# Performance work log

Hardware: AMD Instinct MI355X
Metric: run time of the kernel (lower is better)

## Reference

```python
import jax, jax.numpy as jnp
import numpy as np

N_E = 8192
E_DIM = 256
BETA = 0.25
ORTHO_COEF = 1.0


def setup_inputs() -> dict:
    key = jax.random.key(0)
    k1, k2 = jax.random.split(key)
    z = jax.random.normal(k1, (16, E_DIM, 32, 32), dtype=jnp.float32)
    # nn.Embedding init: uniform(-1/n_e, 1/n_e)
    codebook = jax.random.uniform(k2, (N_E, E_DIM), dtype=jnp.float32,
                                  minval=-1.0 / N_E, maxval=1.0 / N_E)
    return {"z": z, "codebook": codebook}


def reference(z, codebook):
    B, C, H, W = z.shape
    n_e = codebook.shape[0]
    zt = jnp.transpose(z, (0, 2, 3, 1))            # (B,H,W,C)
    zf = zt.reshape(-1, C)                          # (N,C)

    # L2 distances: ||z||^2 + ||e||^2 - 2 z.e
    d = (jnp.sum(zf * zf, axis=1, keepdims=True)
         + jnp.sum(codebook * codebook, axis=1)
         - 2.0 * jnp.matmul(zf, codebook.T))        # (N, n_e)
    idx = jnp.argmin(d, axis=1)                     # (N,)

    z_q_flat = codebook[idx]                        # gather == one-hot @ codebook
    z_q = z_q_flat.reshape(zt.shape)                # (B,H,W,C)

    sg = jax.lax.stop_gradient
    loss = (BETA * jnp.mean((sg(z_q) - zt) ** 2)
            + jnp.mean((z_q - sg(zt)) ** 2))

    # ortho regularizer (force_emb_len_1 == False branch)
    wn = codebook / jnp.linalg.norm(codebook, axis=1, keepdims=True)
    diff = jnp.matmul(wn, wn.T) - jnp.eye(n_e, dtype=codebook.dtype)
    ortho_reg_term = ORTHO_COEF * jnp.sum(diff ** 2) / (n_e ** 2)

    # straight-through estimator
    z_q_st = zt + sg(z_q - zt)

    # perplexity from mean one-hot usage
    N = zf.shape[0]
    counts = jnp.zeros((n_e,), dtype=zt.dtype).at[idx].add(1.0)
    e_mean = counts / N
    perplexity = jnp.exp(-jnp.sum(e_mean * jnp.log(e_mean + 1e-10)))

    z_q_out = jnp.transpose(z_q_st, (0, 3, 1, 2))   # (B,C,H,W)
    return z_q_out, loss, ortho_reg_term, perplexity, idx
```

## Files before the change

### kernel.cpp

```cpp
#include <hip/hip_runtime.h>
#include <hip/hip_bf16.h>
#include <math.h>


#define N_E     8192
#define C_DIM   256
#define N_VEC   16384
#define N_ELEM  4194304
#define MARGIN  6.0e-4f

#define WS_COUNTS   0
#define WS_M        32768
#define WS_ACCUM    294912
#define WS_LISTLEN  294944
#define WS_ZERO_BYTES 295200
#define WS_CE       295200
#define WS_RN       327968
#define WS_A        360736
#define WS_KEYS     426272
#define WS_LISTS    557344
#define WS_TILEMIN  4751648
#define WS_ZBF      8945952
#define WS_CBBF     17334560
#define WS_THR      21528864
#define WS_ZT       21594400

typedef short short8v __attribute__((ext_vector_type(8)));
typedef float f32x4  __attribute__((ext_vector_type(4)));

__device__ inline unsigned short f2bf(float f) {
    unsigned int x = __float_as_uint(f);
    return (unsigned short)((x + 0x7fffu + ((x >> 16) & 1u)) >> 16);
}

__device__ inline void gload16(const void* g, void* l) {
    __builtin_amdgcn_global_load_lds(
        (const __attribute__((address_space(1))) unsigned int*)g,
        (__attribute__((address_space(3))) unsigned int*)l, 16, 0, 0);
}

__global__ __launch_bounds__(256) void k_cbprep(const float* __restrict__ cb,
                                                float* __restrict__ ce,
                                                float* __restrict__ rn,
                                                unsigned short* __restrict__ cbbf) {
    int j = blockIdx.x;
    int tid = threadIdx.x;
    float v = cb[(size_t)j * C_DIM + tid];
    cbbf[(size_t)j * C_DIM + tid] = f2bf(v);
    float s = v * v;
    #pragma unroll
    for (int off = 32; off > 0; off >>= 1) s += __shfl_down(s, off, 64);
    __shared__ float sh[4];
    if ((tid & 63) == 0) sh[tid >> 6] = s;
    __syncthreads();
    if (tid == 0) {
        float t = sh[0] + sh[1] + sh[2] + sh[3];
        ce[j] = t;
        rn[j] = 1.0f / sqrtf(t);
    }
}

__global__ __launch_bounds__(256) void k_ztrans(const float* __restrict__ z,
                                                unsigned short* __restrict__ zbf,
                                                float* __restrict__ zT,
                                                float* __restrict__ A) {
    __shared__ float tile[64 * 260];
    const int tid = threadIdx.x;
    const int n0 = blockIdx.x * 64;
    const int b = n0 >> 10, hw0 = n0 & 1023;
    const float* zp = z + (size_t)b * 262144 + hw0;

    const int hw = tid & 63, cg = tid >> 6;
    #pragma unroll 8
    for (int p = 0; p < 64; ++p) {
        int c = p * 4 + cg;
        tile[hw * 260 + c] = zp[(size_t)c * 1024 + hw];
    }
    __syncthreads();

    if (tid < 64) {
        float a = 0.0f;
        #pragma unroll 8
        for (int c = 0; c < C_DIM; ++c) {
            float v = tile[tid * 260 + c];
            a = fmaf(v, v, a);
        }
        A[n0 + tid] = a;
    }

    const int r = tid >> 2, q = tid & 3;
    unsigned short* dst = zbf + (size_t)(n0 + r) * C_DIM + q * 64;
    float* dstT         = zT  + (size_t)(n0 + r) * C_DIM + q * 64;
    const float* src = &tile[r * 260 + q * 64];
    #pragma unroll
    for (int i = 0; i < 8; ++i) {
        f32x4 lo = *(const f32x4*)&src[i * 8];
        f32x4 hi = *(const f32x4*)&src[i * 8 + 4];
        *(f32x4*)&dstT[i * 8]     = lo;
        *(f32x4*)&dstT[i * 8 + 4] = hi;
        short8v u;
        #pragma unroll
        for (int x = 0; x < 4; ++x) { u[x] = (short)f2bf(lo[x]); u[4 + x] = (short)f2bf(hi[x]); }
        *(short8v*)(dst + i * 8) = u;
    }
}

__global__ __launch_bounds__(256) void k_mfma(const unsigned short* __restrict__ zbf,
                                              const unsigned short* __restrict__ cbbf,
                                              const float* __restrict__ cb,
                                              const float* __restrict__ rn,
                                              float* __restrict__ tilemin,
                                              float* __restrict__ M) {
    __shared__ unsigned long long ldsraw[4352];
    const int tid = threadIdx.x;

    if (blockIdx.x < 8192) {
        unsigned short* As = (unsigned short*)ldsraw;
        unsigned short* Bs = As + 128 * 64;
        float (*smin)[2]   = (float(*)[2])(Bs + 128 * 64);

        const int lin = blockIdx.x;
        const int x = lin & 7, r = lin >> 3;
        const int jp = r >> 7, q = r & 127;
        const int by = x * 16 + (q >> 3), bx = jp * 8 + (q & 7);
        const int n0 = by * 128, j0 = bx * 128;
        const int wave = tid >> 6, lane = tid & 63;
        const int wx = wave & 1, wy = wave >> 1;
        const int g = lane >> 4, c = lane & 15;

        const int lrow  = lane >> 3;
        const int lslot = (lane & 7) ^ lrow;
        const int rbase = wave * 32;

        f32x4 acc[4][4];
        #pragma unroll
        for (int i = 0; i < 4; ++i)
            #pragma unroll
            for (int j = 0; j < 4; ++j) acc[i][j] = (f32x4){0.f, 0.f, 0.f, 0.f};

        for (int kc = 0; kc < C_DIM; kc += 64) {
            __syncthreads();
            #pragma unroll
            for (int i = 0; i < 4; ++i) {
                const int row8 = rbase + i * 8;
                const unsigned short* ga =
                    zbf  + (size_t)(n0 + row8 + lrow) * C_DIM + kc + lslot * 8;
                const unsigned short* gb =
                    cbbf + (size_t)(j0 + row8 + lrow) * C_DIM + kc + lslot * 8;
                gload16(ga, &As[row8 * 64]);
                gload16(gb, &Bs[row8 * 64]);
            }
            __syncthreads();

            #pragma unroll
            for (int kk = 0; kk < 2; ++kk) {
                short8v a[4], b[4];
                #pragma unroll
                for (int f = 0; f < 4; ++f) {
                    const int row = wy * 64 + f * 16 + c;
                    a[f] = *(const short8v*)&As[row * 64 + (((kk * 4 + g) ^ (c & 7)) * 8)];
                }
                #pragma unroll
                for (int f = 0; f < 4; ++f) {
                    const int row = wx * 64 + f * 16 + c;
                    b[f] = *(const short8v*)&Bs[row * 64 + (((kk * 4 + g) ^ (c & 7)) * 8)];
                }
                #pragma unroll
                for (int nf = 0; nf < 4; ++nf)
                    #pragma unroll
                    for (int jf = 0; jf < 4; ++jf)
                        acc[nf][jf] = __builtin_amdgcn_mfma_f32_16x16x32_bf16(
                            a[nf], b[jf], acc[nf][jf], 0, 0, 0);
            }
        }

        #pragma unroll
        for (int nf = 0; nf < 4; ++nf) {
            #pragma unroll
            for (int rr = 0; rr < 4; ++rr) {
                float mx = acc[nf][0][rr];
                #pragma unroll
                for (int jf = 1; jf < 4; ++jf) mx = fmaxf(mx, acc[nf][jf][rr]);
                #pragma unroll
                for (int off = 1; off < 16; off <<= 1)
                    mx = fmaxf(mx, __shfl_xor(mx, off, 64));
                if (c == 0) smin[wy * 64 + nf * 16 + g * 4 + rr][wx] = -2.0f * mx;
            }
        }
        __syncthreads();
        if (tid < 128)
            tilemin[(size_t)bx * N_VEC + n0 + tid] = fminf(smin[tid][0], smin[tid][1]);

    } else {
        float* aT = (float*)ldsraw;
        float* bT = aT + 64 * 68;
        const int gidx = blockIdx.x - 8192;
        const int k0 = (gidx & 3) * 64, l0 = ((gidx >> 2) & 3) * 64;
        const int jc0 = (gidx >> 4) * 256;
        const int tk = tid & 15, tl = tid >> 4;
        float acc[4][4];
        #pragma unroll
        for (int i = 0; i < 4; ++i)
            #pragma unroll
            for (int l = 0; l < 4; ++l) acc[i][l] = 0.0f;

        for (int jc = jc0; jc < jc0 + 256; jc += 64) {
            __syncthreads();
            {
                int kk = tid & 63, jj0 = tid >> 6;
                #pragma unroll
                for (int p = 0; p < 16; ++p) {
                    int jj = p * 4 + jj0;
                    float rr = rn[jc + jj];
                    const float* row = cb + (size_t)(jc + jj) * C_DIM;
                    aT[jj * 68 + kk] = row[k0 + kk] * rr;
                    bT[jj * 68 + kk] = row[l0 + kk] * rr;
                }
            }
            __syncthreads();
            #pragma unroll 8
            for (int jj = 0; jj < 64; ++jj) {
                float4 av = *(const float4*)&aT[jj * 68 + tk * 4];
                float4 bv = *(const float4*)&bT[jj * 68 + tl * 4];
                float a4[4] = {av.x, av.y, av.z, av.w};
                float b4[4] = {bv.x, bv.y, bv.z, bv.w};
                #pragma unroll
                for (int i = 0; i < 4; ++i)
                    #pragma unroll
                    for (int l = 0; l < 4; ++l)
                        acc[i][l] = fmaf(a4[i], b4[l], acc[i][l]);
            }
        }
        #pragma unroll
        for (int i = 0; i < 4; ++i)
            #pragma unroll
            for (int l = 0; l < 4; ++l)
                atomicAdd(&M[(size_t)(k0 + tk * 4 + i) * C_DIM + l0 + tl * 4 + l], acc[i][l]);
    }
}

__global__ __launch_bounds__(256) void k_rowmin(const float* __restrict__ tilemin,
                                               float* __restrict__ thr,
                                               unsigned long long* __restrict__ keys) {
    __shared__ float red[4][64];
    const int nl = threadIdx.x & 63, tg = threadIdx.x >> 6;
    const int n = blockIdx.x * 64 + nl;
    float m = 3.4e38f;
    #pragma unroll
    for (int i = 0; i < 16; ++i)
        m = fminf(m, tilemin[(size_t)(tg * 16 + i) * N_VEC + n]);
    red[tg][nl] = m;
    __syncthreads();
    if (tg == 0) {
        thr[n] = fminf(fminf(red[0][nl], red[1][nl]),
                       fminf(red[2][nl], red[3][nl])) + MARGIN;
        keys[n] = ~0ull;
    }
}

__global__ __launch_bounds__(256) void k_build(const float* __restrict__ tilemin,
                                               const float* __restrict__ thr,
                                               int* __restrict__ listlen,
                                               int* __restrict__ lists) {
    const int t = blockIdx.x;
    const int lane = threadIdx.x & 63;
    #pragma unroll
    for (int it = 0; it < 8; ++it) {
        int n = blockIdx.y * 2048 + it * 256 + threadIdx.x;
        bool qq = tilemin[(size_t)t * N_VEC + n] <= thr[n];
        unsigned long long mask = __ballot(qq);
        if (mask) {
            int ldr = __ffsll(mask) - 1;
            int base = 0;
            if (lane == ldr) base = atomicAdd(&listlen[t], __popcll(mask));
            base = __shfl(base, ldr, 64);
            if (qq) {
                int pre = __popcll(mask & ((1ull << lane) - 1ull));
                lists[t * N_VEC + base + pre] = n;
            }
        }
    }
}

__global__ __launch_bounds__(256) void k_refine2(const float* __restrict__ zT,
                                                 const float* __restrict__ cb,
                                                 const float* __restrict__ ce,
                                                 const float* __restrict__ A,
                                                 const int* __restrict__ listlen,
                                                 const int* __restrict__ lists,
                                                 unsigned long long* __restrict__ keys) {
    __shared__ float e_s[128 * 68];
    __shared__ float z_s[32 * 68];
    __shared__ int   rows_s[32];

    const int t = blockIdx.x;
    const int len = listlen[t];
    const int tid = threadIdx.x;
    const int jg = tid & 31, rg = tid >> 5;
    const int j0 = t * 128;

    for (int b0 = blockIdx.y * 32; b0 < len; b0 += 128 * 32) {
        const int nrows = min(32, len - b0);
        __syncthreads();
        if (tid < 32)
            rows_s[tid] = lists[t * N_VEC + b0 + min(tid, nrows - 1)];

        float acc[4][4];
        #pragma unroll
        for (int rr = 0; rr < 4; ++rr)
            #pragma unroll
            for (int jj = 0; jj < 4; ++jj) acc[rr][jj] = 0.0f;

        for (int kc = 0; kc < C_DIM; kc += 64) {
            __syncthreads();
            {
                int jr = tid >> 1, ko = (tid & 1) * 32;
                #pragma unroll
                for (int i = 0; i < 8; ++i)
                    *(float4*)&e_s[jr * 68 + ko + i * 4] =
                        *(const float4*)&cb[(size_t)(j0 + jr) * C_DIM + kc + ko + i * 4];
            }
            {
                int r = tid >> 3, ko = (tid & 7) * 8;
                const float* zp = &zT[(size_t)rows_s[r] * C_DIM + kc + ko];
                *(float4*)&z_s[r * 68 + ko]     = *(const float4*)&zp[0];
                *(float4*)&z_s[r * 68 + ko + 4] = *(const float4*)&zp[4];
            }
            __syncthreads();

            #pragma unroll
            for (int k4 = 0; k4 < 16; ++k4) {
                float4 ef[4], zf[4];
                #pragma unroll
                for (int jj = 0; jj < 4; ++jj)
                    ef[jj] = *(const float4*)&e_s[(jg + 32 * jj) * 68 + k4 * 4];
                #pragma unroll
                for (int rr = 0; rr < 4; ++rr)
                    zf[rr] = *(const float4*)&z_s[(rg * 4 + rr) * 68 + k4 * 4];
                #pragma unroll
                for (int kk = 0; kk < 4; ++kk)
                    #pragma unroll
                    for (int rr = 0; rr < 4; ++rr)
                        #pragma unroll
                        for (int jj = 0; jj < 4; ++jj)
                            acc[rr][jj] = fmaf(((const float*)&zf[rr])[kk],
                                               ((const float*)&ef[jj])[kk], acc[rr][jj]);
            }
        }

        #pragma unroll
        for (int rr = 0; rr < 4; ++rr) {
            const int n = rows_s[rg * 4 + rr];
            const float An = A[n];
            unsigned long long best = ~0ull;
            #pragma unroll
            for (int jj = 0; jj < 4; ++jj) {
                int j = j0 + jg + 32 * jj;
                float tt = An + ce[j];
                float d = fmaf(-2.0f, acc[rr][jj], tt);
                unsigned int sd = __float_as_uint(d);
                sd = (sd & 0x80000000u) ? ~sd : (sd | 0x80000000u);
                unsigned long long key = ((unsigned long long)sd << 32) | (unsigned)j;
                best = key < best ? key : best;
            }
            #pragma unroll
            for (int off = 16; off > 0; off >>= 1) {
                unsigned long long o = __shfl_xor(best, off, 64);
                best = o < best ? o : best;
            }
            if (jg == 0) atomicMin(&keys[n], best);
        }
    }
}

__global__ __launch_bounds__(256) void k_gather(const float* __restrict__ z,
                                                const float* __restrict__ cb,
                                                const unsigned long long* __restrict__ keys,
                                                float* __restrict__ out,
                                                float* __restrict__ out_idx,
                                                int* __restrict__ counts,
                                                double* __restrict__ sse) {
    int bh = blockIdx.x;
    int b = bh >> 5, h = bh & 31;
    int tid = threadIdx.x;
    __shared__ int sidx[32];
    if (tid < 32) {
        int n = b * 1024 + h * 32 + tid;
        unsigned long long k = keys[n];
        int idx = (int)(k & 0xFFFFFFFFull);
        sidx[tid] = idx;
        out_idx[n] = (float)idx;
        atomicAdd(&counts[idx], 1);
    }
    __syncthreads();
    int w = tid & 31, cy = tid >> 5;
    int jid = sidx[w];
    const float* cbr = cb + (size_t)jid * C_DIM;
    size_t zb = (size_t)b * 262144 + h * 32 + w;

    double acc = 0.0;
    #pragma unroll 4
    for (int cc = 0; cc < 32; ++cc) {
        int c = cc * 8 + cy;
        float e = cbr[c];
        size_t zi = zb + (size_t)c * 1024;
        float d = e - z[zi];
        out[zi] = e;
        acc += (double)(d * d);
    }
    #pragma unroll
    for (int off = 32; off > 0; off >>= 1) acc += __shfl_down(acc, off, 64);
    __shared__ double sh[4];
    if ((tid & 63) == 0) sh[tid >> 6] = acc;
    __syncthreads();
    if (tid == 0) atomicAdd(sse, sh[0] + sh[1] + sh[2] + sh[3]);
}

__global__ __launch_bounds__(256) void k_msq(const float* __restrict__ M,
                                             const int* __restrict__ counts,
                                             double* __restrict__ accum) {
    const int tid = threadIdx.x, bid = blockIdx.x;
    __shared__ double sh[4];
    double s = 0.0;
    if (bid < 64) {
        const float* p = &M[bid * 1024 + tid * 4];
        float4 v = *(const float4*)p;
        s = (double)v.x * v.x + (double)v.y * v.y
          + (double)v.z * v.z + (double)v.w * v.w;
    } else {
        int j = (bid - 64) * 256 + tid;
        double p = counts[j] * (1.0 / (double)N_VEC);
        s = p * log(p + 1e-10);
    }
    #pragma unroll
    for (int off = 32; off > 0; off >>= 1) s += __shfl_down(s, off, 64);
    if ((tid & 63) == 0) sh[tid >> 6] = s;
    __syncthreads();
    if (tid == 0)
        atomicAdd(&accum[bid < 64 ? 1 : 2], sh[0] + sh[1] + sh[2] + sh[3]);
}

__global__ __launch_bounds__(64) void k_final(const double* __restrict__ accum,
                                              float* __restrict__ out_scalars) {
    if (threadIdx.x == 0) {
        out_scalars[0] = (float)(1.25 * accum[0] / (double)N_ELEM);
        out_scalars[1] = (float)((accum[1] - (double)N_E) / ((double)N_E * N_E));
        out_scalars[2] = (float)exp(-accum[2]);
    }
}

extern "C" void kernel_launch(void* const* d_in, const int* in_sizes, int n_in,
                              void* d_out, int out_size, void* d_ws, size_t ws_size,
                              hipStream_t stream) {
    (void)in_sizes; (void)n_in; (void)out_size; (void)ws_size;
    const float* z  = (const float*)d_in[0];
    const float* cb = (const float*)d_in[1];
    float* out = (float*)d_out;

    char* ws = (char*)d_ws;
    int* counts            = (int*)(ws + WS_COUNTS);
    float* M               = (float*)(ws + WS_M);
    double* accum          = (double*)(ws + WS_ACCUM);
    int* listlen           = (int*)(ws + WS_LISTLEN);
    float* ce              = (float*)(ws + WS_CE);
    float* rn              = (float*)(ws + WS_RN);
    float* A               = (float*)(ws + WS_A);
    unsigned long long* keys = (unsigned long long*)(ws + WS_KEYS);
    int* lists             = (int*)(ws + WS_LISTS);
    float* tilemin         = (float*)(ws + WS_TILEMIN);
    unsigned short* zbf    = (unsigned short*)(ws + WS_ZBF);
    unsigned short* cbbf   = (unsigned short*)(ws + WS_CBBF);
    float* thr             = (float*)(ws + WS_THR);
    float* zT              = (float*)(ws + WS_ZT);

    float* out_scalars = out + N_ELEM;
    float* out_idx     = out + N_ELEM + 3;

    hipMemsetAsync(ws, 0, WS_ZERO_BYTES, stream);

    k_cbprep<<<N_E, 256, 0, stream>>>(cb, ce, rn, cbbf);
    k_ztrans<<<N_VEC / 64, 256, 0, stream>>>(z, zbf, zT, A);
    k_mfma<<<8704, 256, 0, stream>>>(zbf, cbbf, cb, rn, tilemin, M);
    k_rowmin<<<N_VEC / 64, 256, 0, stream>>>(tilemin, thr, keys);
    k_build<<<dim3(64, 8), 256, 0, stream>>>(tilemin, thr, listlen, lists);
    k_refine2<<<dim3(64, 128), 256, 0, stream>>>(zT, cb, ce, A, listlen, lists, keys);
    k_gather<<<512, 256, 0, stream>>>(z, cb, keys, out, out_idx, counts, accum);
    k_msq<<<96, 256, 0, stream>>>(M, counts, accum);
    k_final<<<1, 64, 0, stream>>>(accum, out_scalars);
}
```

Baseline: 359.2 us.

## Fuse row-min and candidate list build; split Gram matrix out of MFMA kernel

```diff
diff --git a/kernel.cpp b/kernel.cpp
--- a/kernel.cpp
+++ b/kernel.cpp
@@ -22,8 +22,7 @@
 #define WS_TILEMIN  4751648
 #define WS_ZBF      8945952
 #define WS_CBBF     17334560
-#define WS_THR      21528864
-#define WS_ZT       21594400
+#define WS_ZT       21528864
 
 typedef short short8v __attribute__((ext_vector_type(8)));
 typedef float f32x4  __attribute__((ext_vector_type(4)));
@@ -107,144 +106,94 @@
 
 __global__ __launch_bounds__(256) void k_mfma(const unsigned short* __restrict__ zbf,
                                               const unsigned short* __restrict__ cbbf,
-                                              const float* __restrict__ cb,
-                                              const float* __restrict__ rn,
-                                              float* __restrict__ tilemin,
-                                              float* __restrict__ M) {
-    __shared__ unsigned long long ldsraw[4352];
+                                              float* __restrict__ tilemin) {
+    __shared__ unsigned short As[128 * 64];
+    __shared__ unsigned short Bs[128 * 64];
+    __shared__ float smin[128][2];
+
     const int tid = threadIdx.x;
-
-    if (blockIdx.x < 8192) {
-        unsigned short* As = (unsigned short*)ldsraw;
-        unsigned short* Bs = As + 128 * 64;
-        float (*smin)[2]   = (float(*)[2])(Bs + 128 * 64);
-
-        const int lin = blockIdx.x;
-        const int x = lin & 7, r = lin >> 3;
-        const int jp = r >> 7, q = r & 127;
-        const int by = x * 16 + (q >> 3), bx = jp * 8 + (q & 7);
-        const int n0 = by * 128, j0 = bx * 128;
-        const int wave = tid >> 6, lane = tid & 63;
-        const int wx = wave & 1, wy = wave >> 1;
-        const int g = lane >> 4, c = lane & 15;
-
-        const int lrow  = lane >> 3;
-        const int lslot = (lane & 7) ^ lrow;
-        const int rbase = wave * 32;
-
-        f32x4 acc[4][4];
-        #pragma unroll
-        for (int i = 0; i < 4; ++i)
-            #pragma unroll
-            for (int j = 0; j < 4; ++j) acc[i][j] = (f32x4){0.f, 0.f, 0.f, 0.f};
-
-        for (int kc = 0; kc < C_DIM; kc += 64) {
-            __syncthreads();
-            #pragma unroll
-            for (int i = 0; i < 4; ++i) {
-                const int row8 = rbase + i * 8;
-                const unsigned short* ga =
-                    zbf  + (size_t)(n0 + row8 + lrow) * C_DIM + kc + lslot * 8;
-                const unsigned short* gb =
-                    cbbf + (size_t)(j0 + row8 + lrow) * C_DIM + kc + lslot * 8;
-                gload16(ga, &As[row8 * 64]);
-                gload16(gb, &Bs[row8 * 64]);
-            }
-            __syncthreads();
-
-            #pragma unroll
-            for (int kk = 0; kk < 2; ++kk) {
-                short8v a[4], b[4];
-                #pragma unroll
-                for (int f = 0; f < 4; ++f) {
-                    const int row = wy * 64 + f * 16 + c;
-                    a[f] = *(const short8v*)&As[row * 64 + (((kk * 4 + g) ^ (c & 7)) * 8)];
-                }
-                #pragma unroll
-                for (int f = 0; f < 4; ++f) {
-                    const int row = wx * 64 + f * 16 + c;
-                    b[f] = *(const short8v*)&Bs[row * 64 + (((kk * 4 + g) ^ (c & 7)) * 8)];
-                }
-                #pragma unroll
-                for (int nf = 0; nf < 4; ++nf)
-                    #pragma unroll
-                    for (int jf = 0; jf < 4; ++jf)
-                        acc[nf][jf] = __builtin_amdgcn_mfma_f32_16x16x32_bf16(
-                            a[nf], b[jf], acc[nf][jf], 0, 0, 0);
-            }
-        }
-
-        #pragma unroll
-        for (int nf = 0; nf < 4; ++nf) {
-            #pragma unroll
-            for (int rr = 0; rr < 4; ++rr) {
-                float mx = acc[nf][0][rr];
-                #pragma unroll
-                for (int jf = 1; jf < 4; ++jf) mx = fmaxf(mx, acc[nf][jf][rr]);
-                #pragma unroll
-                for (int off = 1; off < 16; off <<= 1)
-                    mx = fmaxf(mx, __shfl_xor(mx, off, 64));
-                if (c == 0) smin[wy * 64 + nf * 16 + g * 4 + rr][wx] = -2.0f * mx;
-            }
-        }
+    const int lin = blockIdx.x;
+    const int x = lin & 7, r = lin >> 3;
+    const int jp = r >> 7, q = r & 127;
+    const int by = x * 16 + (q >> 3), bx = jp * 8 + (q & 7);
+    const int n0 = by * 128, j0 = bx * 128;
+    const int wave = tid >> 6, lane = tid & 63;
+    const int wx = wave & 1, wy = wave >> 1;
+    const int g = lane >> 4, c = lane & 15;
+
+    const int lrow  = lane >> 3;
+    const int lslot = (lane & 7) ^ lrow;
+    const int rbase = wave * 32;
+
+    f32x4 acc[4][4];
+    #pragma unroll
+    for (int i = 0; i < 4; ++i)
+        #pragma unroll
+        for (int j = 0; j < 4; ++j) acc[i][j] = (f32x4){0.f, 0.f, 0.f, 0.f};
+
+    for (int kc = 0; kc < C_DIM; kc += 64) {
         __syncthreads();
-        if (tid < 128)
-            tilemin[(size_t)bx * N_VEC + n0 + tid] = fminf(smin[tid][0], smin[tid][1]);
-
-    } else {
-        float* aT = (float*)ldsraw;
-        float* bT = aT + 64 * 68;
-        const int gidx = blockIdx.x - 8192;
-        const int k0 = (gidx & 3) * 64, l0 = ((gidx >> 2) & 3) * 64;
-        const int jc0 = (gidx >> 4) * 256;
-        const int tk = tid & 15, tl = tid >> 4;
-        float acc[4][4];
-        #pragma unroll
-        for (int i = 0; i < 4; ++i)
-            #pragma unroll
-            for (int l = 0; l < 4; ++l) acc[i][l] = 0.0f;
-
-        for (int jc = jc0; jc < jc0 + 256; jc += 64) {
-            __syncthreads();
-            {
-                int kk = tid & 63, jj0 = tid >> 6;
-                #pragma unroll
-                for (int p = 0; p < 16; ++p) {
-                    int jj = p * 4 + jj0;
-                    float rr = rn[jc + jj];
-                    const float* row = cb + (size_t)(jc + jj) * C_DIM;
-                    aT[jj * 68 + kk] = row[k0 + kk] * rr;
-                    bT[jj * 68 + kk] = row[l0 + kk] * rr;
-                }
-            }
-            __syncthreads();
-            #pragma unroll 8
-            for (int jj = 0; jj < 64; ++jj) {
-                float4 av = *(const float4*)&aT[jj * 68 + tk * 4];
-                float4 bv = *(const float4*)&bT[jj * 68 + tl * 4];
-                float a4[4] = {av.x, av.y, av.z, av.w};
-                float b4[4] = {bv.x, bv.y, bv.z, bv.w};
-                #pragma unroll
-                for (int i = 0; i < 4; ++i)
-                    #pragma unroll
-                    for (int l = 0; l < 4; ++l)
-                        acc[i][l] = fmaf(a4[i], b4[l], acc[i][l]);
-            }
-        }
-        #pragma unroll
-        for (int i = 0; i < 4; ++i)
-            #pragma unroll
-            for (int l = 0; l < 4; ++l)
-                atomicAdd(&M[(size_t)(k0 + tk * 4 + i) * C_DIM + l0 + tl * 4 + l], acc[i][l]);
-    }
-}
-
-__global__ __launch_bounds__(256) void k_rowmin(const float* __restrict__ tilemin,
-                                               float* __restrict__ thr,
-                                               unsigned long long* __restrict__ keys) {
+        #pragma unroll
+        for (int i = 0; i < 4; ++i) {
+            const int row8 = rbase + i * 8;
+            const unsigned short* ga =
+                zbf  + (size_t)(n0 + row8 + lrow) * C_DIM + kc + lslot * 8;
+            const unsigned short* gb =
+                cbbf + (size_t)(j0 + row8 + lrow) * C_DIM + kc + lslot * 8;
+            gload16(ga, &As[row8 * 64]);
+            gload16(gb, &Bs[row8 * 64]);
+        }
+        __syncthreads();
+
+        #pragma unroll
+        for (int kk = 0; kk < 2; ++kk) {
+            short8v a[4], b[4];
+            #pragma unroll
+            for (int f = 0; f < 4; ++f) {
+                const int row = wy * 64 + f * 16 + c;
+                a[f] = *(const short8v*)&As[row * 64 + (((kk * 4 + g) ^ (c & 7)) * 8)];
+            }
+            #pragma unroll
+            for (int f = 0; f < 4; ++f) {
+                const int row = wx * 64 + f * 16 + c;
+                b[f] = *(const short8v*)&Bs[row * 64 + (((kk * 4 + g) ^ (c & 7)) * 8)];
+            }
+            #pragma unroll
+            for (int nf = 0; nf < 4; ++nf)
+                #pragma unroll
+                for (int jf = 0; jf < 4; ++jf)
+                    acc[nf][jf] = __builtin_amdgcn_mfma_f32_16x16x32_bf16(
+                        a[nf], b[jf], acc[nf][jf], 0, 0, 0);
+        }
+    }
+
+    #pragma unroll
+    for (int nf = 0; nf < 4; ++nf) {
+        #pragma unroll
+        for (int rr = 0; rr < 4; ++rr) {
+            float mx = acc[nf][0][rr];
+            #pragma unroll
+            for (int jf = 1; jf < 4; ++jf) mx = fmaxf(mx, acc[nf][jf][rr]);
+            #pragma unroll
+            for (int off = 1; off < 16; off <<= 1)
+                mx = fmaxf(mx, __shfl_xor(mx, off, 64));
+            if (c == 0) smin[wy * 64 + nf * 16 + g * 4 + rr][wx] = -2.0f * mx;
+        }
+    }
+    __syncthreads();
+    if (tid < 128)
+        tilemin[(size_t)bx * N_VEC + n0 + tid] = fminf(smin[tid][0], smin[tid][1]);
+}
+
+__global__ __launch_bounds__(256) void k_cand2(const float* __restrict__ tilemin,
+                                               unsigned long long* __restrict__ keys,
+                                               int* __restrict__ listlen,
+                                               int* __restrict__ lists) {
     __shared__ float red[4][64];
+    __shared__ float thr_s[64];
     const int nl = threadIdx.x & 63, tg = threadIdx.x >> 6;
     const int n = blockIdx.x * 64 + nl;
+
     float m = 3.4e38f;
     #pragma unroll
     for (int i = 0; i < 16; ++i)
@@ -252,30 +201,25 @@
     red[tg][nl] = m;
     __syncthreads();
     if (tg == 0) {
-        thr[n] = fminf(fminf(red[0][nl], red[1][nl]),
-                       fminf(red[2][nl], red[3][nl])) + MARGIN;
+        thr_s[nl] = fminf(fminf(red[0][nl], red[1][nl]),
+                          fminf(red[2][nl], red[3][nl])) + MARGIN;
         keys[n] = ~0ull;
     }
-}
-
-__global__ __launch_bounds__(256) void k_build(const float* __restrict__ tilemin,
-                                               const float* __restrict__ thr,
-                                               int* __restrict__ listlen,
-                                               int* __restrict__ lists) {
-    const int t = blockIdx.x;
-    const int lane = threadIdx.x & 63;
-    #pragma unroll
-    for (int it = 0; it < 8; ++it) {
-        int n = blockIdx.y * 2048 + it * 256 + threadIdx.x;
-        bool qq = tilemin[(size_t)t * N_VEC + n] <= thr[n];
+    __syncthreads();
+    const float thr = thr_s[nl];
+
+    #pragma unroll
+    for (int i = 0; i < 16; ++i) {
+        const int t = tg * 16 + i;
+        bool qq = tilemin[(size_t)t * N_VEC + n] <= thr;
         unsigned long long mask = __ballot(qq);
         if (mask) {
             int ldr = __ffsll(mask) - 1;
             int base = 0;
-            if (lane == ldr) base = atomicAdd(&listlen[t], __popcll(mask));
+            if (nl == ldr) base = atomicAdd(&listlen[t], __popcll(mask));
             base = __shfl(base, ldr, 64);
             if (qq) {
-                int pre = __popcll(mask & ((1ull << lane) - 1ull));
+                int pre = __popcll(mask & ((1ull << nl) - 1ull));
                 lists[t * N_VEC + base + pre] = n;
             }
         }
@@ -416,6 +360,55 @@
     if (tid == 0) atomicAdd(sse, sh[0] + sh[1] + sh[2] + sh[3]);
 }
 
+__global__ __launch_bounds__(256) void k_gram(const float* __restrict__ cb,
+                                              const float* __restrict__ rn,
+                                              float* __restrict__ M) {
+    __shared__ float aT[64][68];
+    __shared__ float bT[64][68];
+    int k0 = blockIdx.x * 64, l0 = blockIdx.y * 64;
+    int jc0 = blockIdx.z * 256;
+    int tid = threadIdx.x;
+    int tk = tid & 15, tl = tid >> 4;
+    float acc[4][4];
+    #pragma unroll
+    for (int i = 0; i < 4; ++i)
+        #pragma unroll
+        for (int l = 0; l < 4; ++l) acc[i][l] = 0.0f;
+
+    for (int jc = jc0; jc < jc0 + 256; jc += 64) {
+        __syncthreads();
+        {
+            int kk = tid & 63, jj0 = tid >> 6;
+            #pragma unroll
+            for (int p = 0; p < 16; ++p) {
+                int jj = p * 4 + jj0;
+                float r = rn[jc + jj];
+                const float* row = cb + (size_t)(jc + jj) * C_DIM;
+                aT[jj][kk] = row[k0 + kk] * r;
+                bT[jj][kk] = row[l0 + kk] * r;
+            }
+        }
+        __syncthreads();
+        #pragma unroll 8
+        for (int jj = 0; jj < 64; ++jj) {
+            float4 av = *(const float4*)&aT[jj][tk * 4];
+            float4 bv = *(const float4*)&bT[jj][tl * 4];
+            float a4[4] = {av.x, av.y, av.z, av.w};
+            float b4[4] = {bv.x, bv.y, bv.z, bv.w};
+            #pragma unroll
+            for (int i = 0; i < 4; ++i)
+                #pragma unroll
+                for (int l = 0; l < 4; ++l)
+                    acc[i][l] = fmaf(a4[i], b4[l], acc[i][l]);
+        }
+    }
+    #pragma unroll
+    for (int i = 0; i < 4; ++i)
+        #pragma unroll
+        for (int l = 0; l < 4; ++l)
+            atomicAdd(&M[(size_t)(k0 + tk * 4 + i) * C_DIM + l0 + tl * 4 + l], acc[i][l]);
+}
+
 __global__ __launch_bounds__(256) void k_msq(const float* __restrict__ M,
                                              const int* __restrict__ counts,
                                              double* __restrict__ accum) {
@@ -470,7 +463,6 @@
     float* tilemin         = (float*)(ws + WS_TILEMIN);
     unsigned short* zbf    = (unsigned short*)(ws + WS_ZBF);
     unsigned short* cbbf   = (unsigned short*)(ws + WS_CBBF);
-    float* thr             = (float*)(ws + WS_THR);
     float* zT              = (float*)(ws + WS_ZT);
 
     float* out_scalars = out + N_ELEM;
@@ -480,11 +472,11 @@
 
     k_cbprep<<<N_E, 256, 0, stream>>>(cb, ce, rn, cbbf);
     k_ztrans<<<N_VEC / 64, 256, 0, stream>>>(z, zbf, zT, A);
-    k_mfma<<<8704, 256, 0, stream>>>(zbf, cbbf, cb, rn, tilemin, M);
-    k_rowmin<<<N_VEC / 64, 256, 0, stream>>>(tilemin, thr, keys);
-    k_build<<<dim3(64, 8), 256, 0, stream>>>(tilemin, thr, listlen, lists);
+    k_mfma<<<8192, 256, 0, stream>>>(zbf, cbbf, tilemin);
+    k_cand2<<<N_VEC / 64, 256, 0, stream>>>(tilemin, keys, listlen, lists);
     k_refine2<<<dim3(64, 128), 256, 0, stream>>>(zT, cb, ce, A, listlen, lists, keys);
     k_gather<<<512, 256, 0, stream>>>(z, cb, keys, out, out_idx, counts, accum);
+    k_gram<<<dim3(4, 4, 32), 256, 0, stream>>>(cb, rn, M);
     k_msq<<<96, 256, 0, stream>>>(M, counts, accum);
     k_final<<<1, 64, 0, stream>>>(accum, out_scalars);
 }
```

Measured after the change: 343.1 us. 1.05x faster.
